# Kernel tuning notes

Measured on AMD Instinct MI355X. Metric: run time of the kernel, lower is better.

The kernel has to match this reference:

```python
import jax, jax.numpy as jnp
import numpy as np

RANK = 16
ALPHA = 16.0
SCALING = ALPHA / RANK
N_ADAPTERS = 8


def setup_inputs() -> dict:
    key = jax.random.key(0)
    k_x, k_a, k_b, k_id = jax.random.split(key, 4)
    b, n, d_in, d_out = 8, 1024, 2048, 2048
    x = jax.random.normal(k_x, (b, n, d_in), dtype=jnp.float32)
    A = jax.random.normal(k_a, (N_ADAPTERS, d_out, RANK), dtype=jnp.float32) * 0.02
    B = jax.random.normal(k_b, (N_ADAPTERS, RANK, d_in), dtype=jnp.float32)
    adapter_ids = jax.random.randint(k_id, (b,), 0, N_ADAPTERS, dtype=jnp.int32)
    return {"x": x, "A": A, "B": B, "adapter_ids": adapter_ids}


def reference(x, A, B, adapter_ids):
    # Bx: [b, n, a, r] = einsum over in_features
    Bx = jnp.einsum('bni,ari->bnar', x, B)
    # result: [b, n, a, o]
    result = jnp.einsum('bnar,aor->bnao', Bx, A)
    # per-sample adapter gather: out[b, n, o] = result[b, n, adapter_ids[b], :]
    bidx = jnp.arange(x.shape[0])
    out = result[bidx, :, adapter_ids, :]  # [b, n, o]
    return out * SCALING  # dropout p=0.0 is identity
```

## Files before the change

kernel.cpp:

```cpp
#include <hip/hip_runtime.h>
#include <hip/hip_bf16.h>

#define RANK    16
#define D_IN    2048
#define D_OUT   2048
#define N_TOK   1024
#define N_BATCH 8
#define TPB     16
#define SCALING 1.0f

__device__ __forceinline__ float dot4(float4 a, float4 b) {
    return a.x * b.x + a.y * b.y + a.z * b.z + a.w * b.w;
}

__global__ __launch_bounds__(256, 2)
void lora_fused(const float* __restrict__ x,
                const float* __restrict__ A,
                const float* __restrict__ B,
                const int* __restrict__ ids,
                float* __restrict__ out) {
    __shared__ __align__(16) float Bt[RANK][512];
    __shared__ __align__(16) float bx[TPB][RANK];

    const int b    = blockIdx.y;
    const int tok0 = blockIdx.x * TPB;
    const int aid  = ids[b];
    const int tid  = threadIdx.x;
    const int wave = tid >> 6;
    const int lane = tid & 63;

    const float* __restrict__ xb = x + ((size_t)b * N_TOK + tok0) * D_IN;
    const float* __restrict__ Ba = B + (size_t)aid * RANK * D_IN;
    const float* __restrict__ Aa = A + (size_t)aid * D_OUT * RANK;
    float* __restrict__ ob = out + ((size_t)b * N_TOK + tok0) * D_OUT;

    float acc[4][RANK];
    #pragma unroll
    for (int t = 0; t < 4; ++t)
        #pragma unroll
        for (int r = 0; r < RANK; ++r) acc[t][r] = 0.f;

    for (int tile = 0; tile < 4; ++tile) {
        __syncthreads();
        #pragma unroll
        for (int k = 0; k < 8; ++k) {
            int flat = (k * 256 + tid) * 4;
            int r = flat >> 9;
            int c = flat & 511;
            *reinterpret_cast<float4*>(&Bt[r][c]) =
                *reinterpret_cast<const float4*>(&Ba[r * D_IN + tile * 512 + c]);
        }
        __syncthreads();

        #pragma unroll
        for (int t = 0; t < 4; ++t) {
            const float* xr = xb + (size_t)(wave * 4 + t) * D_IN + tile * 512;
            #pragma unroll
            for (int it = 0; it < 2; ++it) {
                int il = it * 256 + lane * 4;
                float4 xv = *reinterpret_cast<const float4*>(&xr[il]);
                #pragma unroll
                for (int r = 0; r < RANK; ++r) {
                    float4 bv = *reinterpret_cast<const float4*>(&Bt[r][il]);
                    acc[t][r] += dot4(xv, bv);
                }
            }
        }
    }

    #pragma unroll
    for (int t = 0; t < 4; ++t) {
        #pragma unroll
        for (int r = 0; r < RANK; ++r) {
            float v = acc[t][r];
            #pragma unroll
            for (int off = 32; off > 0; off >>= 1)
                v += __shfl_xor(v, off, 64);
            acc[t][r] = v;
        }
        if (lane == 0) {
            int tt = wave * 4 + t;
            *reinterpret_cast<float4*>(&bx[tt][0])  = make_float4(acc[t][0],  acc[t][1],  acc[t][2],  acc[t][3]);
            *reinterpret_cast<float4*>(&bx[tt][4])  = make_float4(acc[t][4],  acc[t][5],  acc[t][6],  acc[t][7]);
            *reinterpret_cast<float4*>(&bx[tt][8])  = make_float4(acc[t][8],  acc[t][9],  acc[t][10], acc[t][11]);
            *reinterpret_cast<float4*>(&bx[tt][12]) = make_float4(acc[t][12], acc[t][13], acc[t][14], acc[t][15]);
        }
    }
    __syncthreads();

    #pragma unroll
    for (int it = 0; it < 2; ++it) {
        int o0 = wave * 512 + it * 256 + lane * 4;
        float4 Ar[4][4];
        #pragma unroll
        for (int oo = 0; oo < 4; ++oo)
            #pragma unroll
            for (int q = 0; q < 4; ++q)
                Ar[oo][q] = *reinterpret_cast<const float4*>(&Aa[(size_t)(o0 + oo) * RANK + q * 4]);

        #pragma unroll
        for (int t = 0; t < TPB; ++t) {
            float4 b0 = *reinterpret_cast<const float4*>(&bx[t][0]);
            float4 b1 = *reinterpret_cast<const float4*>(&bx[t][4]);
            float4 b2 = *reinterpret_cast<const float4*>(&bx[t][8]);
            float4 b3 = *reinterpret_cast<const float4*>(&bx[t][12]);
            float4 res;
            res.x = dot4(Ar[0][0], b0) + dot4(Ar[0][1], b1) + dot4(Ar[0][2], b2) + dot4(Ar[0][3], b3);
            res.y = dot4(Ar[1][0], b0) + dot4(Ar[1][1], b1) + dot4(Ar[1][2], b2) + dot4(Ar[1][3], b3);
            res.z = dot4(Ar[2][0], b0) + dot4(Ar[2][1], b1) + dot4(Ar[2][2], b2) + dot4(Ar[2][3], b3);
            res.w = dot4(Ar[3][0], b0) + dot4(Ar[3][1], b1) + dot4(Ar[3][2], b2) + dot4(Ar[3][3], b3);
            res.x *= SCALING; res.y *= SCALING; res.z *= SCALING; res.w *= SCALING;
            *reinterpret_cast<float4*>(&ob[(size_t)t * D_OUT + o0]) = res;
        }
    }
}

extern "C" void kernel_launch(void* const* d_in, const int* in_sizes, int n_in,
                              void* d_out, int out_size, void* d_ws, size_t ws_size,
                              hipStream_t stream) {
    const float* x   = (const float*)d_in[0];
    const float* A   = (const float*)d_in[1];
    const float* B   = (const float*)d_in[2];
    const int*   ids = (const int*)d_in[3];
    float* out = (float*)d_out;

    dim3 grid(N_TOK / TPB, N_BATCH);
    lora_fused<<<grid, 256, 0, stream>>>(x, A, B, ids, out);
}
```

Baseline: 143.4 us.

## Split rank across waves, keep B in registers, drop shared-memory B staging

Each wave now owns 4 of the 16 rank rows and reads its B rows straight from global memory into registers, while all 8 tokens per block are processed by every wave. This removes the shared-memory B tile and its per-tile barriers, and halves tokens per block to raise occupancy (launch bounds 4). The cross-lane reduction uses DPP ops for the first stages. In exchange, x rows are now read by all four waves (more L1/L2 traffic), and the grid doubles, so the A reads in the second stage are repeated for twice as many blocks.

```diff
diff --git a/kernel.cpp b/kernel.cpp
--- a/kernel.cpp
+++ b/kernel.cpp
@@ -1,26 +1,39 @@
 #include <hip/hip_runtime.h>
-#include <hip/hip_bf16.h>
 
-#define RANK    16
-#define D_IN    2048
-#define D_OUT   2048
-#define N_TOK   1024
-#define N_BATCH 8
-#define TPB     16
-#define SCALING 1.0f
+#define D_IN   2048
+#define D_OUT  2048
+#define N_TOK  1024
+#define N_B    8
+#define RANK   16
+#define TPB    8
 
 __device__ __forceinline__ float dot4(float4 a, float4 b) {
     return a.x * b.x + a.y * b.y + a.z * b.z + a.w * b.w;
 }
 
-__global__ __launch_bounds__(256, 2)
-void lora_fused(const float* __restrict__ x,
-                const float* __restrict__ A,
-                const float* __restrict__ B,
-                const int* __restrict__ ids,
-                float* __restrict__ out) {
-    __shared__ __align__(16) float Bt[RANK][512];
-    __shared__ __align__(16) float bx[TPB][RANK];
+template <int CTRL>
+__device__ __forceinline__ float dpp_add(float v) {
+    int s = __builtin_amdgcn_update_dpp(0, __float_as_int(v), CTRL, 0xF, 0xF, true);
+    return v + __int_as_float(s);
+}
+
+__device__ __forceinline__ float wave_sum(float v) {
+    v = dpp_add<0xB1>(v);
+    v = dpp_add<0x4E>(v);
+    v = dpp_add<0x124>(v);
+    v = dpp_add<0x128>(v);
+    v += __shfl_xor(v, 16, 64);
+    v += __shfl_xor(v, 32, 64);
+    return v;
+}
+
+__global__ __launch_bounds__(256, 4)
+void lora_fused_v2(const float* __restrict__ x,
+                   const float* __restrict__ A,
+                   const float* __restrict__ B,
+                   const int* __restrict__ ids,
+                   float* __restrict__ out) {
+    __shared__ __align__(16) float bxs[TPB][RANK];
 
     const int b    = blockIdx.y;
     const int tok0 = blockIdx.x * TPB;
@@ -30,86 +43,71 @@
     const int lane = tid & 63;
 
     const float* __restrict__ xb = x + ((size_t)b * N_TOK + tok0) * D_IN;
-    const float* __restrict__ Ba = B + (size_t)aid * RANK * D_IN;
+    const float* __restrict__ Ba = B + (size_t)aid * RANK * D_IN + (size_t)(wave * 4) * D_IN;
     const float* __restrict__ Aa = A + (size_t)aid * D_OUT * RANK;
     float* __restrict__ ob = out + ((size_t)b * N_TOK + tok0) * D_OUT;
 
-    float acc[4][RANK];
+    float acc[TPB][4];
     #pragma unroll
-    for (int t = 0; t < 4; ++t)
+    for (int t = 0; t < TPB; ++t)
         #pragma unroll
-        for (int r = 0; r < RANK; ++r) acc[t][r] = 0.f;
+        for (int r = 0; r < 4; ++r) acc[t][r] = 0.f;
 
+    #pragma unroll
     for (int tile = 0; tile < 4; ++tile) {
-        __syncthreads();
         #pragma unroll
-        for (int k = 0; k < 8; ++k) {
-            int flat = (k * 256 + tid) * 4;
-            int r = flat >> 9;
-            int c = flat & 511;
-            *reinterpret_cast<float4*>(&Bt[r][c]) =
-                *reinterpret_cast<const float4*>(&Ba[r * D_IN + tile * 512 + c]);
-        }
-        __syncthreads();
-
-        #pragma unroll
-        for (int t = 0; t < 4; ++t) {
-            const float* xr = xb + (size_t)(wave * 4 + t) * D_IN + tile * 512;
+        for (int it = 0; it < 2; ++it) {
+            const int ib = tile * 512 + it * 256 + lane * 4;
+            const float4 b0 = *reinterpret_cast<const float4*>(&Ba[0 * D_IN + ib]);
+            const float4 b1 = *reinterpret_cast<const float4*>(&Ba[1 * D_IN + ib]);
+            const float4 b2 = *reinterpret_cast<const float4*>(&Ba[2 * D_IN + ib]);
+            const float4 b3 = *reinterpret_cast<const float4*>(&Ba[3 * D_IN + ib]);
             #pragma unroll
-            for (int it = 0; it < 2; ++it) {
-                int il = it * 256 + lane * 4;
-                float4 xv = *reinterpret_cast<const float4*>(&xr[il]);
-                #pragma unroll
-                for (int r = 0; r < RANK; ++r) {
-                    float4 bv = *reinterpret_cast<const float4*>(&Bt[r][il]);
-                    acc[t][r] += dot4(xv, bv);
-                }
+            for (int t = 0; t < TPB; ++t) {
+                const float4 xv = *reinterpret_cast<const float4*>(&xb[(size_t)t * D_IN + ib]);
+                acc[t][0] += dot4(xv, b0);
+                acc[t][1] += dot4(xv, b1);
+                acc[t][2] += dot4(xv, b2);
+                acc[t][3] += dot4(xv, b3);
             }
         }
     }
 
     #pragma unroll
-    for (int t = 0; t < 4; ++t) {
+    for (int t = 0; t < TPB; ++t)
         #pragma unroll
-        for (int r = 0; r < RANK; ++r) {
-            float v = acc[t][r];
-            #pragma unroll
-            for (int off = 32; off > 0; off >>= 1)
-                v += __shfl_xor(v, off, 64);
-            acc[t][r] = v;
-        }
-        if (lane == 0) {
-            int tt = wave * 4 + t;
-            *reinterpret_cast<float4*>(&bx[tt][0])  = make_float4(acc[t][0],  acc[t][1],  acc[t][2],  acc[t][3]);
-            *reinterpret_cast<float4*>(&bx[tt][4])  = make_float4(acc[t][4],  acc[t][5],  acc[t][6],  acc[t][7]);
-            *reinterpret_cast<float4*>(&bx[tt][8])  = make_float4(acc[t][8],  acc[t][9],  acc[t][10], acc[t][11]);
-            *reinterpret_cast<float4*>(&bx[tt][12]) = make_float4(acc[t][12], acc[t][13], acc[t][14], acc[t][15]);
-        }
+        for (int r = 0; r < 4; ++r)
+            acc[t][r] = wave_sum(acc[t][r]);
+
+    if (lane == 0) {
+        #pragma unroll
+        for (int t = 0; t < TPB; ++t)
+            *reinterpret_cast<float4*>(&bxs[t][wave * 4]) =
+                make_float4(acc[t][0], acc[t][1], acc[t][2], acc[t][3]);
     }
     __syncthreads();
 
     #pragma unroll
-    for (int it = 0; it < 2; ++it) {
-        int o0 = wave * 512 + it * 256 + lane * 4;
+    for (int half = 0; half < 2; ++half) {
+        const int o0 = half * 1024 + tid * 4;
         float4 Ar[4][4];
         #pragma unroll
-        for (int oo = 0; oo < 4; ++oo)
+        for (int j = 0; j < 4; ++j)
             #pragma unroll
             for (int q = 0; q < 4; ++q)
-                Ar[oo][q] = *reinterpret_cast<const float4*>(&Aa[(size_t)(o0 + oo) * RANK + q * 4]);
+                Ar[j][q] = *reinterpret_cast<const float4*>(&Aa[(size_t)(o0 + j) * RANK + q * 4]);
 
         #pragma unroll
         for (int t = 0; t < TPB; ++t) {
-            float4 b0 = *reinterpret_cast<const float4*>(&bx[t][0]);
-            float4 b1 = *reinterpret_cast<const float4*>(&bx[t][4]);
-            float4 b2 = *reinterpret_cast<const float4*>(&bx[t][8]);
-            float4 b3 = *reinterpret_cast<const float4*>(&bx[t][12]);
+            const float4 p0 = *reinterpret_cast<const float4*>(&bxs[t][0]);
+            const float4 p1 = *reinterpret_cast<const float4*>(&bxs[t][4]);
+            const float4 p2 = *reinterpret_cast<const float4*>(&bxs[t][8]);
+            const float4 p3 = *reinterpret_cast<const float4*>(&bxs[t][12]);
             float4 res;
-            res.x = dot4(Ar[0][0], b0) + dot4(Ar[0][1], b1) + dot4(Ar[0][2], b2) + dot4(Ar[0][3], b3);
-            res.y = dot4(Ar[1][0], b0) + dot4(Ar[1][1], b1) + dot4(Ar[1][2], b2) + dot4(Ar[1][3], b3);
-            res.z = dot4(Ar[2][0], b0) + dot4(Ar[2][1], b1) + dot4(Ar[2][2], b2) + dot4(Ar[2][3], b3);
-            res.w = dot4(Ar[3][0], b0) + dot4(Ar[3][1], b1) + dot4(Ar[3][2], b2) + dot4(Ar[3][3], b3);
-            res.x *= SCALING; res.y *= SCALING; res.z *= SCALING; res.w *= SCALING;
+            res.x = dot4(Ar[0][0], p0) + dot4(Ar[0][1], p1) + dot4(Ar[0][2], p2) + dot4(Ar[0][3], p3);
+            res.y = dot4(Ar[1][0], p0) + dot4(Ar[1][1], p1) + dot4(Ar[1][2], p2) + dot4(Ar[1][3], p3);
+            res.z = dot4(Ar[2][0], p0) + dot4(Ar[2][1], p1) + dot4(Ar[2][2], p2) + dot4(Ar[2][3], p3);
+            res.w = dot4(Ar[3][0], p0) + dot4(Ar[3][1], p1) + dot4(Ar[3][2], p2) + dot4(Ar[3][3], p3);
             *reinterpret_cast<float4*>(&ob[(size_t)t * D_OUT + o0]) = res;
         }
     }
@@ -124,6 +122,6 @@
     const int*   ids = (const int*)d_in[3];
     float* out = (float*)d_out;
 
-    dim3 grid(N_TOK / TPB, N_BATCH);
-    lora_fused<<<grid, 256, 0, stream>>>(x, A, B, ids, out);
+    dim3 grid(N_TOK / TPB, N_B);
+    lora_fused_v2<<<grid, 256, 0, stream>>>(x, A, B, ids, out);
 }
```

Result: slower. 394.6 us (+175.2%).
